# Optimization experiments

Hardware: AMD Instinct MI355X
Metric: run time of the kernel (lower is better)

The kernel has to match this reference:

```python
import jax, jax.numpy as jnp
import numpy as np

D = 384      # ViT-S feature dim (feat_dim_lookup['s'])
H = 6        # module forces num_heads = 6
L = 12       # ViT-S depth
RATIO = 0.1  # attention_mask_ratio
EPS = 1e-6


def layernorm(x, g, b):
    m = x.mean(-1, keepdims=True)
    v = ((x - m) ** 2).mean(-1, keepdims=True)
    return (x - m) * jax.lax.rsqrt(v + EPS) * g + b


def masked_attn(x, w_qkv, b_qkv, w_o, b_o):
    # Patch._fix_attn_masking: full softmax attention, threshold at ratio*row_max, renormalize.
    B, N, Dm = x.shape
    dh = Dm // H
    qkv = (x @ w_qkv + b_qkv).reshape(B, N, 3, H, dh)
    q = qkv[:, :, 0].transpose(0, 2, 1, 3)  # [B,H,N,dh]
    k = qkv[:, :, 1].transpose(0, 2, 1, 3)
    v = qkv[:, :, 2].transpose(0, 2, 1, 3)
    scores = jnp.einsum('bhqd,bhkd->bhqk', q, k) * (dh ** -0.5)
    attn = jax.nn.softmax(scores, axis=-1)
    thresh = RATIO * attn.max(axis=-1, keepdims=True)
    attn = jnp.where(attn >= thresh, attn, 0.0)
    attn = attn / attn.sum(axis=-1, keepdims=True)  # re-normalize
    out = jnp.einsum('bhqk,bhkd->bhqd', attn, v)
    out = out.transpose(0, 2, 1, 3).reshape(B, N, Dm)
    return out @ w_o + b_o, attn


def block(x, p):
    w_qkv, b_qkv, w_o, b_o, g1, be1, g2, be2, w1, b1, w2, b2 = p
    h, attn = masked_attn(layernorm(x, g1, be1), w_qkv, b_qkv, w_o, b_o)
    x = x + h
    h = layernorm(x, g2, be2) @ w1 + b1
    h = jax.nn.gelu(h, approximate=False) @ w2 + b2
    return x + h, attn


def setup_inputs() -> dict:
    key = jax.random.key(0)
    ks = jax.random.split(key, 8)
    B, N = 2, 962  # 2 transforms; (1+(160-8)//5)**2 + 1 cls = 962 tokens
    s = 0.02
    return {
        'x': jax.random.normal(ks[0], (B, N, D), jnp.float32),
        'w_qkv': jax.random.normal(ks[1], (L, D, 3 * D), jnp.float32) * s,
        'b_qkv': jnp.zeros((L, 3 * D), jnp.float32),
        'w_proj': jax.random.normal(ks[2], (L, D, D), jnp.float32) * s,
        'b_proj': jnp.zeros((L, D), jnp.float32),
        'ln1_g': jnp.ones((L, D), jnp.float32),
        'ln1_b': jnp.zeros((L, D), jnp.float32),
        'ln2_g': jnp.ones((L, D), jnp.float32),
        'ln2_b': jnp.zeros((L, D), jnp.float32),
        'w_fc1': jax.random.normal(ks[3], (L, D, 4 * D), jnp.float32) * s,
        'b_fc1': jnp.zeros((L, 4 * D), jnp.float32),
        'w_fc2': jax.random.normal(ks[4], (L, 4 * D, D), jnp.float32) * s,
        'b_fc2': jnp.zeros((L, D), jnp.float32),
        'lnf_g': jnp.ones((D,), jnp.float32),
        'lnf_b': jnp.zeros((D,), jnp.float32),
    }


def reference(x, w_qkv, b_qkv, w_proj, b_proj, ln1_g, ln1_b, ln2_g, ln2_b,
              w_fc1, b_fc1, w_fc2, b_fc2, lnf_g, lnf_b):
    params = (w_qkv, b_qkv, w_proj, b_proj, ln1_g, ln1_b, ln2_g, ln2_b,
              w_fc1, b_fc1, w_fc2, b_fc2)
    first = jax.tree_util.tree_map(lambda a: a[:-1], params)
    last = jax.tree_util.tree_map(lambda a: a[-1], params)

    def scan_fn(h, p):
        h, _ = block(h, p)
        return h, None

    x, _ = jax.lax.scan(scan_fn, x, first)  # blocks 0..L-2
    x, attn = block(x, last)                # last block, keep masked attention
    feats = layernorm(x, lnf_g, lnf_b)      # [B, N, D]
    return feats, attn
```

## Files before the change

kernel.cpp:

```cpp
#include <hip/hip_runtime.h>
#include <hip/hip_bf16.h>
#include <math.h>

typedef __bf16 bf16_t;
typedef __bf16 bf16x8 __attribute__((ext_vector_type(8)));
typedef __bf16 bf16x2 __attribute__((ext_vector_type(2)));
typedef float f32x4 __attribute__((ext_vector_type(4)));
typedef float f32x16 __attribute__((ext_vector_type(16)));

#define NEGBIG -3.0e38f

__global__ void __launch_bounds__(256) trall_k(
    const float* __restrict__ w_qkv, const float* __restrict__ w_proj,
    const float* __restrict__ w_fc1, const float* __restrict__ w_fc2,
    bf16_t* __restrict__ wt_qkv, bf16_t* __restrict__ wt_proj,
    bf16_t* __restrict__ wt_fc1, bf16_t* __restrict__ wt_fc2)
{
    __shared__ float T[32][33];
    int t = blockIdx.x;
    int z = t / 1728, r = t % 1728;
    const float* W; bf16_t* Wt; int K, N, n0, k0;
    if (r < 432)       { W = w_qkv;  Wt = wt_qkv;  K = 384;  N = 1152; n0 = (r % 36) * 32;               k0 = (r / 36) * 32; }
    else if (r < 576)  { W = w_proj; Wt = wt_proj; K = 384;  N = 384;  int rr = r - 432;  n0 = (rr % 12) * 32; k0 = (rr / 12) * 32; }
    else if (r < 1152) { W = w_fc1;  Wt = wt_fc1;  K = 384;  N = 1536; int rr = r - 576;  n0 = (rr % 48) * 32; k0 = (rr / 48) * 32; }
    else               { W = w_fc2;  Wt = wt_fc2;  K = 1536; N = 384;  int rr = r - 1152; n0 = (rr % 12) * 32; k0 = (rr / 12) * 32; }
    const float* Wl = W + (size_t)z * K * N;
    bf16_t* Wtl = Wt + (size_t)z * K * N;
    int tx = threadIdx.x & 31, ty = threadIdx.x >> 5;
#pragma unroll
    for (int i = 0; i < 4; ++i)
        T[ty + 8 * i][tx] = Wl[(size_t)(k0 + ty + 8 * i) * N + n0 + tx];
    __syncthreads();
#pragma unroll
    for (int i = 0; i < 4; ++i)
        Wtl[(size_t)(n0 + ty + 8 * i) * K + k0 + tx] = (bf16_t)T[tx][ty + 8 * i];
}

__global__ void __launch_bounds__(256) lncopy_k(
    const float* __restrict__ xin, const float* __restrict__ g,
    const float* __restrict__ b, float* __restrict__ xf,
    bf16_t* __restrict__ out)
{
    int t = blockIdx.x * 4 + (threadIdx.x >> 6);
    int lane = threadIdx.x & 63;
    const float* xp = xin + (size_t)t * 384;
    float v[6];
    float s = 0.f;
#pragma unroll
    for (int i = 0; i < 6; ++i) { v[i] = xp[lane + 64 * i]; s += v[i]; }
#pragma unroll
    for (int i = 0; i < 6; ++i) xf[(size_t)t * 384 + lane + 64 * i] = v[i];
    for (int off = 32; off > 0; off >>= 1) s += __shfl_xor(s, off);
    float mean = s * (1.0f / 384.0f);
    float s2 = 0.f;
#pragma unroll
    for (int i = 0; i < 6; ++i) { float d = v[i] - mean; s2 += d * d; }
    for (int off = 32; off > 0; off >>= 1) s2 += __shfl_xor(s2, off);
    float rstd = rsqrtf(s2 * (1.0f / 384.0f) + 1e-6f);
#pragma unroll
    for (int i = 0; i < 6; ++i) {
        int c = lane + 64 * i;
        out[(size_t)t * 384 + c] = (bf16_t)((v[i] - mean) * rstd * g[c] + b[c]);
    }
}

template <int NP, typename OT, bool WX>
__global__ void __launch_bounds__(256) ln_red_k(
    const float* __restrict__ x, const float* __restrict__ part,
    const float* __restrict__ g, const float* __restrict__ b,
    float* __restrict__ xupd, OT* __restrict__ out)
{
    int t = blockIdx.x * 4 + (threadIdx.x >> 6);
    int lane = threadIdx.x & 63;
    const size_t base = (size_t)t * 384;
    float v[6];
#pragma unroll
    for (int i = 0; i < 6; ++i) v[i] = x[base + lane + 64 * i];
#pragma unroll
    for (int p = 0; p < NP; ++p)
#pragma unroll
        for (int i = 0; i < 6; ++i)
            v[i] += part[(size_t)p * 738816 + base + lane + 64 * i];
    float s = 0.f;
#pragma unroll
    for (int i = 0; i < 6; ++i) {
        if (WX) xupd[base + lane + 64 * i] = v[i];
        s += v[i];
    }
    for (int off = 32; off > 0; off >>= 1) s += __shfl_xor(s, off);
    float mean = s * (1.0f / 384.0f);
    float s2 = 0.f;
#pragma unroll
    for (int i = 0; i < 6; ++i) { float d = v[i] - mean; s2 += d * d; }
    for (int off = 32; off > 0; off >>= 1) s2 += __shfl_xor(s2, off);
    float rstd = rsqrtf(s2 * (1.0f / 384.0f) + 1e-6f);
#pragma unroll
    for (int i = 0; i < 6; ++i) {
        int c = lane + 64 * i;
        out[base + c] = (OT)((v[i] - mean) * rstd * g[c] + b[c]);
    }
}

template <int MODE>
__global__ void __launch_bounds__(256) gemm_k(
    const bf16_t* __restrict__ A, const bf16_t* __restrict__ Bt,
    const float* __restrict__ bias, int M, int N, int K,
    bf16_t* __restrict__ outb,
    bf16_t* __restrict__ qb, bf16_t* __restrict__ kb, bf16_t* __restrict__ vtb)
{
    __shared__ alignas(16) bf16_t As[2][64][72];
    __shared__ alignas(16) bf16_t Bs[2][64][72];

    const int tid  = threadIdx.x;
    const int wave = tid >> 6, lane = tid & 63;
    const int m0 = blockIdx.y * 64, n0 = blockIdx.x * 64;
    const int rb = (wave >> 1) * 32, cb = (wave & 1) * 32;
    const int r32 = lane & 31, half = lane >> 5;
    const int h8 = half * 8;

    const int lrow = tid >> 3;
    const int lcol = (tid & 7) * 8;

    const bf16_t* pA0 = A  + (size_t)(m0 + lrow) * K + lcol;
    const bf16_t* pA1 = pA0 + (size_t)32 * K;
    const bf16_t* pB0 = Bt + (size_t)(n0 + lrow) * K + lcol;
    const bf16_t* pB1 = pB0 + (size_t)32 * K;

    f32x16 acc = {};
    bf16x8 va0, va1, vb0, vb1;

    va0 = *(const bf16x8*)(pA0);
    va1 = *(const bf16x8*)(pA1);
    vb0 = *(const bf16x8*)(pB0);
    vb1 = *(const bf16x8*)(pB1);
    *(bf16x8*)(&As[0][lrow][lcol])      = va0;
    *(bf16x8*)(&As[0][lrow + 32][lcol]) = va1;
    *(bf16x8*)(&Bs[0][lrow][lcol])      = vb0;
    *(bf16x8*)(&Bs[0][lrow + 32][lcol]) = vb1;

    int cur = 0;
    for (int k0 = 0; k0 < K; k0 += 64) {
        __syncthreads();
        const bool has_next = (k0 + 64 < K);
        if (has_next) {
            va0 = *(const bf16x8*)(pA0 + k0 + 64);
            va1 = *(const bf16x8*)(pA1 + k0 + 64);
            vb0 = *(const bf16x8*)(pB0 + k0 + 64);
            vb1 = *(const bf16x8*)(pB1 + k0 + 64);
        }
#pragma unroll
        for (int kc = 0; kc < 64; kc += 16) {
            bf16x8 a = *(const bf16x8*)(&As[cur][rb + r32][kc + h8]);
            bf16x8 b = *(const bf16x8*)(&Bs[cur][cb + r32][kc + h8]);
            acc = __builtin_amdgcn_mfma_f32_32x32x16_bf16(a, b, acc, 0, 0, 0);
        }
        if (has_next) {
            int nxt = cur ^ 1;
            *(bf16x8*)(&As[nxt][lrow][lcol])      = va0;
            *(bf16x8*)(&As[nxt][lrow + 32][lcol]) = va1;
            *(bf16x8*)(&Bs[nxt][lrow][lcol])      = vb0;
            *(bf16x8*)(&Bs[nxt][lrow + 32][lcol]) = vb1;
            cur = nxt;
        }
    }

    const int gc = n0 + cb + r32;
    const float bv = bias[gc];
    if (MODE == 2) {
#pragma unroll
        for (int reg = 0; reg < 16; ++reg) {
            int gr = m0 + rb + (reg & 3) + 8 * (reg >> 2) + 4 * half;
            if (gr >= M) continue;
            float val = acc[reg] + bv;
            float g = 0.5f * val * (1.0f + erff(val * 0.70710678118654752f));
            outb[(size_t)gr * N + gc] = (bf16_t)g;
        }
    } else {
        const int which = n0 / 384;
        if (which < 2) {
            const int rem = gc % 384;
            const int h = rem >> 6, d = rem & 63;
#pragma unroll
            for (int reg = 0; reg < 16; ++reg) {
                int gr = m0 + rb + (reg & 3) + 8 * (reg >> 2) + 4 * half;
                if (gr >= M) continue;
                float val = acc[reg] + bv;
                int bb = (gr >= 962) ? 1 : 0;
                int n = gr - 962 * bb;
                int bh = bb * 6 + h;
                bf16_t bvv = (bf16_t)val;
                if (which == 0) qb[((size_t)bh * 962 + n) * 64 + d] = bvv;
                else            kb[((size_t)bh * 962 + n) * 64 + d] = bvv;
            }
        } else {
            bf16_t (*T)[66] = (bf16_t (*)[66])(&As[0][0][0]);
            const int hh = (n0 - 768) >> 6;
            __syncthreads();
#pragma unroll
            for (int reg = 0; reg < 16; ++reg) {
                int rl = rb + (reg & 3) + 8 * (reg >> 2) + 4 * half;
                T[rl][cb + r32] = (bf16_t)(acc[reg] + bv);
            }
            __syncthreads();
            const int dl  = (wave << 4) + (lane >> 3);
            const int ncs = (lane & 7) * 8;
#pragma unroll
            for (int h8v = 0; h8v < 2; ++h8v) {
                int d = dl + h8v * 8;
                int ng0 = m0 + ncs;
                if (ng0 >= 1924) continue;
                bf16x8 v8;
#pragma unroll
                for (int j = 0; j < 8; ++j) v8[j] = T[ncs + j][d];
                int bb0 = (ng0 >= 962), bb7 = ((ng0 + 7) >= 962);
                if (bb0 == bb7 && ng0 + 7 < 1924) {
                    size_t off = ((size_t)(bb0 * 6 + hh) * 64 + d) * 992 + (ng0 - 962 * bb0);
                    if (bb0 == 0) {
                        *(bf16x8*)(vtb + off) = v8;
                    } else {
                        bf16x2* d2 = (bf16x2*)(vtb + off);
#pragma unroll
                        for (int j2 = 0; j2 < 4; ++j2) {
                            bf16x2 t2; t2[0] = v8[2 * j2]; t2[1] = v8[2 * j2 + 1];
                            d2[j2] = t2;
                        }
                    }
                } else {
                    for (int j = 0; j < 8; ++j) {
                        int ng = ng0 + j;
                        if (ng >= 1924) break;
                        int bb = (ng >= 962);
                        vtb[((size_t)(bb * 6 + hh) * 64 + d) * 992 + ng - 962 * bb] = v8[j];
                    }
                }
            }
        }
    }
}

template <int KLEN>
__global__ void __launch_bounds__(256) gemm_sp(
    const bf16_t* __restrict__ A, int lda,
    const bf16_t* __restrict__ Bt, int ldb,
    const float* __restrict__ bias, int M, int N,
    float* __restrict__ part)
{
    __shared__ alignas(16) bf16_t As[2][64][72];
    __shared__ alignas(16) bf16_t Bs[2][64][72];

    const int tid  = threadIdx.x;
    const int wave = tid >> 6, lane = tid & 63;
    const int m0 = blockIdx.y * 64, n0 = blockIdx.x * 64;
    const int rb = (wave >> 1) * 32, cb = (wave & 1) * 32;
    const int r32 = lane & 31, half = lane >> 5;
    const int h8 = half * 8;
    const int ks = blockIdx.z * KLEN;

    const int lrow = tid >> 3;
    const int lcol = (tid & 7) * 8;

    const bf16_t* pA0 = A  + (size_t)(m0 + lrow) * lda + ks + lcol;
    const bf16_t* pA1 = pA0 + (size_t)32 * lda;
    const bf16_t* pB0 = Bt + (size_t)(n0 + lrow) * ldb + ks + lcol;
    const bf16_t* pB1 = pB0 + (size_t)32 * ldb;

    f32x16 acc = {};
    bf16x8 va0, va1, vb0, vb1;

    va0 = *(const bf16x8*)(pA0);
    va1 = *(const bf16x8*)(pA1);
    vb0 = *(const bf16x8*)(pB0);
    vb1 = *(const bf16x8*)(pB1);
    *(bf16x8*)(&As[0][lrow][lcol])      = va0;
    *(bf16x8*)(&As[0][lrow + 32][lcol]) = va1;
    *(bf16x8*)(&Bs[0][lrow][lcol])      = vb0;
    *(bf16x8*)(&Bs[0][lrow + 32][lcol]) = vb1;

    int cur = 0;
    for (int k0 = 0; k0 < KLEN; k0 += 64) {
        __syncthreads();
        const bool has_next = (k0 + 64 < KLEN);
        if (has_next) {
            va0 = *(const bf16x8*)(pA0 + k0 + 64);
            va1 = *(const bf16x8*)(pA1 + k0 + 64);
            vb0 = *(const bf16x8*)(pB0 + k0 + 64);
            vb1 = *(const bf16x8*)(pB1 + k0 + 64);
        }
#pragma unroll
        for (int kc = 0; kc < 64; kc += 16) {
            bf16x8 a = *(const bf16x8*)(&As[cur][rb + r32][kc + h8]);
            bf16x8 b = *(const bf16x8*)(&Bs[cur][cb + r32][kc + h8]);
            acc = __builtin_amdgcn_mfma_f32_32x32x16_bf16(a, b, acc, 0, 0, 0);
        }
        if (has_next) {
            int nxt = cur ^ 1;
            *(bf16x8*)(&As[nxt][lrow][lcol])      = va0;
            *(bf16x8*)(&As[nxt][lrow + 32][lcol]) = va1;
            *(bf16x8*)(&Bs[nxt][lrow][lcol])      = vb0;
            *(bf16x8*)(&Bs[nxt][lrow + 32][lcol]) = vb1;
            cur = nxt;
        }
    }

    const int gc = n0 + cb + r32;
    const float bv = (blockIdx.z == 0) ? bias[gc] : 0.f;
    float* pz = part + (size_t)blockIdx.z * 738816;
#pragma unroll
    for (int reg = 0; reg < 16; ++reg) {
        int gr = m0 + rb + (reg & 3) + 8 * (reg >> 2) + 4 * half;
        if (gr >= M) continue;
        pz[(size_t)gr * N + gc] = acc[reg] + bv;
    }
}

__global__ void __launch_bounds__(256) attn_k(
    const bf16_t* __restrict__ qb, const bf16_t* __restrict__ kb,
    const bf16_t* __restrict__ vtb, bf16_t* __restrict__ attnout,
    float* __restrict__ attn_save)
{
    __shared__ alignas(16) bf16_t S[16][1000];

    const int tid  = threadIdx.x;
    const int wave = tid >> 6, lane = tid & 63;
    const int q4 = lane >> 4, mm = lane & 15;
    const int bh = blockIdx.y, qt = blockIdx.x;
    const int qrow0 = qt * 16;

    int qr = qrow0 + mm; if (qr > 961) qr = 961;
    const bf16_t* qptr = qb + ((size_t)bh * 962 + qr) * 64 + q4 * 8;
    bf16x8 aq0 = *(const bf16x8*)(qptr);
    bf16x8 aq1 = *(const bf16x8*)(qptr + 32);

    for (int ct = wave; ct < 61; ct += 4) {
        int kr = ct * 16 + mm; if (kr > 961) kr = 961;
        const bf16_t* kptr = kb + ((size_t)bh * 962 + kr) * 64 + q4 * 8;
        bf16x8 b0 = *(const bf16x8*)(kptr);
        bf16x8 b1 = *(const bf16x8*)(kptr + 32);
        f32x4 acc = {};
        acc = __builtin_amdgcn_mfma_f32_16x16x32_bf16(aq0, b0, acc, 0, 0, 0);
        acc = __builtin_amdgcn_mfma_f32_16x16x32_bf16(aq1, b1, acc, 0, 0, 0);
        int col = ct * 16 + mm;
#pragma unroll
        for (int r = 0; r < 4; ++r) {
            int row = q4 * 4 + r;
            if (col < 962) S[row][col] = (bf16_t)(acc[r] * 0.125f);
        }
    }
    for (int idx = tid; idx < 16 * 38; idx += 256) {
        int r = idx / 38, c = 962 + idx % 38;
        S[r][c] = (bf16_t)NEGBIG;
    }
    __syncthreads();

    const int trow = tid >> 4, ti = tid & 15;
    float e[8][8];
    float mx = NEGBIG;
#pragma unroll
    for (int t = 0; t < 8; ++t) {
        int c8 = ti * 8 + 128 * t;
        bf16x8 xv;
        if (c8 < 1000) xv = *(const bf16x8*)(&S[trow][c8]);
        else {
#pragma unroll
            for (int j = 0; j < 8; ++j) xv[j] = (bf16_t)NEGBIG;
        }
#pragma unroll
        for (int j = 0; j < 8; ++j) { e[t][j] = (float)xv[j]; mx = fmaxf(mx, e[t][j]); }
    }
#pragma unroll
    for (int off = 8; off > 0; off >>= 1) mx = fmaxf(mx, __shfl_xor(mx, off, 16));

    float sum = 0.f;
#pragma unroll
    for (int t = 0; t < 8; ++t)
#pragma unroll
    for (int j = 0; j < 8; ++j) {
        float ev = __expf(e[t][j] - mx);
        e[t][j] = ev;
        if (ev >= 0.1f) sum += ev;
    }
#pragma unroll
    for (int off = 8; off > 0; off >>= 1) sum += __shfl_xor(sum, off, 16);
    float inv = 1.0f / sum;

    int row_g = qrow0 + trow;
#pragma unroll
    for (int t = 0; t < 8; ++t) {
        int c8 = ti * 8 + 128 * t;
        if (c8 >= 1000) continue;
        bf16x8 pv;
#pragma unroll
        for (int j = 0; j < 8; ++j) {
            float pp = (e[t][j] >= 0.1f) ? e[t][j] * inv : 0.f;
            e[t][j] = pp;
            pv[j] = (bf16_t)pp;
        }
        *(bf16x8*)(&S[trow][c8]) = pv;
        if (attn_save && row_g < 962) {
#pragma unroll
            for (int j = 0; j < 8; ++j)
                if (c8 + j < 962)
                    attn_save[((size_t)bh * 962 + row_g) * 962 + c8 + j] = e[t][j];
        }
    }
    __syncthreads();

    const int wc0 = wave * 16;
    f32x4 o = {};
    for (int kc = 0; kc < 31; ++kc) {
        bf16x8 pa = *(const bf16x8*)(&S[mm][kc * 32 + q4 * 8]);
        bf16x8 vb = *(const bf16x8*)(vtb + ((size_t)bh * 64 + wc0 + mm) * 992 + kc * 32 + q4 * 8);
        o = __builtin_amdgcn_mfma_f32_16x16x32_bf16(pa, vb, o, 0, 0, 0);
    }
    int b = bh / 6, h = bh % 6;
#pragma unroll
    for (int r = 0; r < 4; ++r) {
        int qrr = qrow0 + q4 * 4 + r;
        if (qrr < 962)
            attnout[((size_t)(b * 962 + qrr)) * 384 + h * 64 + wc0 + mm] = (bf16_t)o[r];
    }
}

extern "C" void kernel_launch(void* const* d_in, const int* in_sizes, int n_in,
                              void* d_out, int out_size, void* d_ws, size_t ws_size,
                              hipStream_t stream)
{
    const float* xin    = (const float*)d_in[0];
    const float* w_qkv  = (const float*)d_in[1];
    const float* b_qkv  = (const float*)d_in[2];
    const float* w_proj = (const float*)d_in[3];
    const float* b_proj = (const float*)d_in[4];
    const float* ln1g   = (const float*)d_in[5];
    const float* ln1b   = (const float*)d_in[6];
    const float* ln2g   = (const float*)d_in[7];
    const float* ln2b   = (const float*)d_in[8];
    const float* w_fc1  = (const float*)d_in[9];
    const float* b_fc1  = (const float*)d_in[10];
    const float* w_fc2  = (const float*)d_in[11];
    const float* b_fc2  = (const float*)d_in[12];
    const float* lnfg   = (const float*)d_in[13];
    const float* lnfb   = (const float*)d_in[14];

    float* feats     = (float*)d_out;
    float* attn_save = feats + 738816;

    char* p = (char*)d_ws;
    auto alloc = [&](size_t bytes) {
        char* r = p;
        p += (bytes + 255) & ~(size_t)255;
        return r;
    };
    float*  x_f32   = (float*)alloc(1924ull * 384 * 4);
    bf16_t* xn      = (bf16_t*)alloc(1984ull * 384 * 2);
    bf16_t* qbuf    = (bf16_t*)alloc(12ull * 962 * 64 * 2);
    bf16_t* kbuf    = (bf16_t*)alloc(12ull * 962 * 64 * 2);
    bf16_t* vtbuf   = (bf16_t*)alloc(12ull * 64 * 992 * 2);
    bf16_t* attnout = (bf16_t*)alloc(1984ull * 384 * 2);
    bf16_t* mlp1    = (bf16_t*)alloc(1984ull * 1536 * 2);
    bf16_t* wt_qkv  = (bf16_t*)alloc(12ull * 1152 * 384 * 2);
    bf16_t* wt_proj = (bf16_t*)alloc(12ull * 384 * 384 * 2);
    bf16_t* wt_fc1  = (bf16_t*)alloc(12ull * 1536 * 384 * 2);
    bf16_t* wt_fc2  = (bf16_t*)alloc(12ull * 384 * 1536 * 2);
    float*  partbuf = (float*)alloc(4ull * 1924 * 384 * 4);

    trall_k<<<dim3(20736), dim3(256), 0, stream>>>(
        w_qkv, w_proj, w_fc1, w_fc2, wt_qkv, wt_proj, wt_fc1, wt_fc2);

    lncopy_k<<<dim3(481), dim3(256), 0, stream>>>(xin, ln1g, ln1b, x_f32, xn);

    for (int l = 0; l < 12; ++l) {
        gemm_k<0><<<dim3(18, 31), dim3(256), 0, stream>>>(
            xn, wt_qkv + (size_t)l * 1152 * 384, b_qkv + l * 1152,
            1924, 1152, 384, nullptr, qbuf, kbuf, vtbuf);
        attn_k<<<dim3(61, 12), dim3(256), 0, stream>>>(
            qbuf, kbuf, vtbuf, attnout, (l == 11) ? attn_save : (float*)nullptr);
        gemm_sp<192><<<dim3(6, 31, 2), dim3(256), 0, stream>>>(
            attnout, 384, wt_proj + (size_t)l * 384 * 384, 384, b_proj + l * 384,
            1924, 384, partbuf);
        ln_red_k<2, bf16_t, true><<<dim3(481), dim3(256), 0, stream>>>(
            x_f32, partbuf, ln2g + l * 384, ln2b + l * 384, x_f32, xn);
        gemm_k<2><<<dim3(24, 31), dim3(256), 0, stream>>>(
            xn, wt_fc1 + (size_t)l * 1536 * 384, b_fc1 + l * 1536,
            1924, 1536, 384, mlp1, nullptr, nullptr, nullptr);
        gemm_sp<384><<<dim3(6, 31, 4), dim3(256), 0, stream>>>(
            mlp1, 1536, wt_fc2 + (size_t)l * 384 * 1536, 1536, b_fc2 + l * 384,
            1924, 384, partbuf);
        if (l < 11) {
            ln_red_k<4, bf16_t, true><<<dim3(481), dim3(256), 0, stream>>>(
                x_f32, partbuf, ln1g + (l + 1) * 384, ln1b + (l + 1) * 384, x_f32, xn);
        } else {
            ln_red_k<4, float, false><<<dim3(481), dim3(256), 0, stream>>>(
                x_f32, partbuf, lnfg, lnfb, x_f32, feats);
        }
    }
}
```

Measured before the change: 966.0 us.

## Merge prep kernels, deepen GEMM register prefetch, vectorize attention-save stores

Folds the initial layernorm-copy kernel into the weight transpose kernel as extra blocks, saving one launch. Both GEMM kernels now prefetch global tiles two K-steps ahead using double register buffers, which gives loads more time to land behind the MFMA work. The attention-probability save in the last layer writes float pairs instead of scalars. The deeper prefetch raises register pressure, and the pair stores depend on row alignment, which holds because 962 is even.

```diff
diff --git a/kernel.cpp b/kernel.cpp
--- a/kernel.cpp
+++ b/kernel.cpp
@@ -5,17 +5,46 @@
 typedef __bf16 bf16_t;
 typedef __bf16 bf16x8 __attribute__((ext_vector_type(8)));
 typedef __bf16 bf16x2 __attribute__((ext_vector_type(2)));
+typedef float f32x2 __attribute__((ext_vector_type(2)));
 typedef float f32x4 __attribute__((ext_vector_type(4)));
 typedef float f32x16 __attribute__((ext_vector_type(16)));
 
 #define NEGBIG -3.0e38f
 
-__global__ void __launch_bounds__(256) trall_k(
+__global__ void __launch_bounds__(256) prep_k(
     const float* __restrict__ w_qkv, const float* __restrict__ w_proj,
     const float* __restrict__ w_fc1, const float* __restrict__ w_fc2,
     bf16_t* __restrict__ wt_qkv, bf16_t* __restrict__ wt_proj,
-    bf16_t* __restrict__ wt_fc1, bf16_t* __restrict__ wt_fc2)
+    bf16_t* __restrict__ wt_fc1, bf16_t* __restrict__ wt_fc2,
+    const float* __restrict__ xin, const float* __restrict__ g,
+    const float* __restrict__ b, float* __restrict__ xf,
+    bf16_t* __restrict__ xnout)
 {
+    if (blockIdx.x >= 20736) {
+        int t = (blockIdx.x - 20736) * 4 + (threadIdx.x >> 6);
+        int lane = threadIdx.x & 63;
+        const float* xp = xin + (size_t)t * 384;
+        float v[6];
+        float s = 0.f;
+#pragma unroll
+        for (int i = 0; i < 6; ++i) { v[i] = xp[lane + 64 * i]; s += v[i]; }
+#pragma unroll
+        for (int i = 0; i < 6; ++i) xf[(size_t)t * 384 + lane + 64 * i] = v[i];
+        for (int off = 32; off > 0; off >>= 1) s += __shfl_xor(s, off);
+        float mean = s * (1.0f / 384.0f);
+        float s2 = 0.f;
+#pragma unroll
+        for (int i = 0; i < 6; ++i) { float d = v[i] - mean; s2 += d * d; }
+        for (int off = 32; off > 0; off >>= 1) s2 += __shfl_xor(s2, off);
+        float rstd = rsqrtf(s2 * (1.0f / 384.0f) + 1e-6f);
+#pragma unroll
+        for (int i = 0; i < 6; ++i) {
+            int c = lane + 64 * i;
+            xnout[(size_t)t * 384 + c] = (bf16_t)((v[i] - mean) * rstd * g[c] + b[c]);
+        }
+        return;
+    }
+
     __shared__ float T[32][33];
     int t = blockIdx.x;
     int z = t / 1728, r = t % 1728;
@@ -36,34 +65,6 @@
         Wtl[(size_t)(n0 + ty + 8 * i) * K + k0 + tx] = (bf16_t)T[tx][ty + 8 * i];
 }
 
-__global__ void __launch_bounds__(256) lncopy_k(
-    const float* __restrict__ xin, const float* __restrict__ g,
-    const float* __restrict__ b, float* __restrict__ xf,
-    bf16_t* __restrict__ out)
-{
-    int t = blockIdx.x * 4 + (threadIdx.x >> 6);
-    int lane = threadIdx.x & 63;
-    const float* xp = xin + (size_t)t * 384;
-    float v[6];
-    float s = 0.f;
-#pragma unroll
-    for (int i = 0; i < 6; ++i) { v[i] = xp[lane + 64 * i]; s += v[i]; }
-#pragma unroll
-    for (int i = 0; i < 6; ++i) xf[(size_t)t * 384 + lane + 64 * i] = v[i];
-    for (int off = 32; off > 0; off >>= 1) s += __shfl_xor(s, off);
-    float mean = s * (1.0f / 384.0f);
-    float s2 = 0.f;
-#pragma unroll
-    for (int i = 0; i < 6; ++i) { float d = v[i] - mean; s2 += d * d; }
-    for (int off = 32; off > 0; off >>= 1) s2 += __shfl_xor(s2, off);
-    float rstd = rsqrtf(s2 * (1.0f / 384.0f) + 1e-6f);
-#pragma unroll
-    for (int i = 0; i < 6; ++i) {
-        int c = lane + 64 * i;
-        out[(size_t)t * 384 + c] = (bf16_t)((v[i] - mean) * rstd * g[c] + b[c]);
-    }
-}
-
 template <int NP, typename OT, bool WX>
 __global__ void __launch_bounds__(256) ln_red_k(
     const float* __restrict__ x, const float* __restrict__ part,
@@ -127,26 +128,33 @@
     const bf16_t* pB1 = pB0 + (size_t)32 * K;
 
     f32x16 acc = {};
-    bf16x8 va0, va1, vb0, vb1;
-
-    va0 = *(const bf16x8*)(pA0);
-    va1 = *(const bf16x8*)(pA1);
-    vb0 = *(const bf16x8*)(pB0);
-    vb1 = *(const bf16x8*)(pB1);
-    *(bf16x8*)(&As[0][lrow][lcol])      = va0;
-    *(bf16x8*)(&As[0][lrow + 32][lcol]) = va1;
-    *(bf16x8*)(&Bs[0][lrow][lcol])      = vb0;
-    *(bf16x8*)(&Bs[0][lrow + 32][lcol]) = vb1;
+    bf16x8 va0[2], va1[2], vb0[2], vb1[2];
+
+    va0[0] = *(const bf16x8*)(pA0);
+    va1[0] = *(const bf16x8*)(pA1);
+    vb0[0] = *(const bf16x8*)(pB0);
+    vb1[0] = *(const bf16x8*)(pB1);
+    if (64 < K) {
+        va0[1] = *(const bf16x8*)(pA0 + 64);
+        va1[1] = *(const bf16x8*)(pA1 + 64);
+        vb0[1] = *(const bf16x8*)(pB0 + 64);
+        vb1[1] = *(const bf16x8*)(pB1 + 64);
+    }
+    *(bf16x8*)(&As[0][lrow][lcol])      = va0[0];
+    *(bf16x8*)(&As[0][lrow + 32][lcol]) = va1[0];
+    *(bf16x8*)(&Bs[0][lrow][lcol])      = vb0[0];
+    *(bf16x8*)(&Bs[0][lrow + 32][lcol]) = vb1[0];
 
     int cur = 0;
-    for (int k0 = 0; k0 < K; k0 += 64) {
+    int i = 0;
+    for (int k0 = 0; k0 < K; k0 += 64, ++i) {
         __syncthreads();
-        const bool has_next = (k0 + 64 < K);
-        if (has_next) {
-            va0 = *(const bf16x8*)(pA0 + k0 + 64);
-            va1 = *(const bf16x8*)(pA1 + k0 + 64);
-            vb0 = *(const bf16x8*)(pB0 + k0 + 64);
-            vb1 = *(const bf16x8*)(pB1 + k0 + 64);
+        const int s = i & 1;
+        if (k0 + 128 < K) {
+            va0[s] = *(const bf16x8*)(pA0 + k0 + 128);
+            va1[s] = *(const bf16x8*)(pA1 + k0 + 128);
+            vb0[s] = *(const bf16x8*)(pB0 + k0 + 128);
+            vb1[s] = *(const bf16x8*)(pB1 + k0 + 128);
         }
 #pragma unroll
         for (int kc = 0; kc < 64; kc += 16) {
@@ -154,12 +162,13 @@
             bf16x8 b = *(const bf16x8*)(&Bs[cur][cb + r32][kc + h8]);
             acc = __builtin_amdgcn_mfma_f32_32x32x16_bf16(a, b, acc, 0, 0, 0);
         }
-        if (has_next) {
+        if (k0 + 64 < K) {
+            const int ns = s ^ 1;
             int nxt = cur ^ 1;
-            *(bf16x8*)(&As[nxt][lrow][lcol])      = va0;
-            *(bf16x8*)(&As[nxt][lrow + 32][lcol]) = va1;
-            *(bf16x8*)(&Bs[nxt][lrow][lcol])      = vb0;
-            *(bf16x8*)(&Bs[nxt][lrow + 32][lcol]) = vb1;
+            *(bf16x8*)(&As[nxt][lrow][lcol])      = va0[ns];
+            *(bf16x8*)(&As[nxt][lrow + 32][lcol]) = va1[ns];
+            *(bf16x8*)(&Bs[nxt][lrow][lcol])      = vb0[ns];
+            *(bf16x8*)(&Bs[nxt][lrow + 32][lcol]) = vb1[ns];
             cur = nxt;
         }
     }
@@ -265,26 +274,33 @@
     const bf16_t* pB1 = pB0 + (size_t)32 * ldb;
 
     f32x16 acc = {};
-    bf16x8 va0, va1, vb0, vb1;
-
-    va0 = *(const bf16x8*)(pA0);
-    va1 = *(const bf16x8*)(pA1);
-    vb0 = *(const bf16x8*)(pB0);
-    vb1 = *(const bf16x8*)(pB1);
-    *(bf16x8*)(&As[0][lrow][lcol])      = va0;
-    *(bf16x8*)(&As[0][lrow + 32][lcol]) = va1;
-    *(bf16x8*)(&Bs[0][lrow][lcol])      = vb0;
-    *(bf16x8*)(&Bs[0][lrow + 32][lcol]) = vb1;
+    bf16x8 va0[2], va1[2], vb0[2], vb1[2];
+
+    va0[0] = *(const bf16x8*)(pA0);
+    va1[0] = *(const bf16x8*)(pA1);
+    vb0[0] = *(const bf16x8*)(pB0);
+    vb1[0] = *(const bf16x8*)(pB1);
+    if (64 < KLEN) {
+        va0[1] = *(const bf16x8*)(pA0 + 64);
+        va1[1] = *(const bf16x8*)(pA1 + 64);
+        vb0[1] = *(const bf16x8*)(pB0 + 64);
+        vb1[1] = *(const bf16x8*)(pB1 + 64);
+    }
+    *(bf16x8*)(&As[0][lrow][lcol])      = va0[0];
+    *(bf16x8*)(&As[0][lrow + 32][lcol]) = va1[0];
+    *(bf16x8*)(&Bs[0][lrow][lcol])      = vb0[0];
+    *(bf16x8*)(&Bs[0][lrow + 32][lcol]) = vb1[0];
 
     int cur = 0;
-    for (int k0 = 0; k0 < KLEN; k0 += 64) {
+    int i = 0;
+    for (int k0 = 0; k0 < KLEN; k0 += 64, ++i) {
         __syncthreads();
-        const bool has_next = (k0 + 64 < KLEN);
-        if (has_next) {
-            va0 = *(const bf16x8*)(pA0 + k0 + 64);
-            va1 = *(const bf16x8*)(pA1 + k0 + 64);
-            vb0 = *(const bf16x8*)(pB0 + k0 + 64);
-            vb1 = *(const bf16x8*)(pB1 + k0 + 64);
+        const int s = i & 1;
+        if (k0 + 128 < KLEN) {
+            va0[s] = *(const bf16x8*)(pA0 + k0 + 128);
+            va1[s] = *(const bf16x8*)(pA1 + k0 + 128);
+            vb0[s] = *(const bf16x8*)(pB0 + k0 + 128);
+            vb1[s] = *(const bf16x8*)(pB1 + k0 + 128);
         }
 #pragma unroll
         for (int kc = 0; kc < 64; kc += 16) {
@@ -292,12 +308,13 @@
             bf16x8 b = *(const bf16x8*)(&Bs[cur][cb + r32][kc + h8]);
             acc = __builtin_amdgcn_mfma_f32_32x32x16_bf16(a, b, acc, 0, 0, 0);
         }
-        if (has_next) {
+        if (k0 + 64 < KLEN) {
+            const int ns = s ^ 1;
             int nxt = cur ^ 1;
-            *(bf16x8*)(&As[nxt][lrow][lcol])      = va0;
-            *(bf16x8*)(&As[nxt][lrow + 32][lcol]) = va1;
-            *(bf16x8*)(&Bs[nxt][lrow][lcol])      = vb0;
-            *(bf16x8*)(&Bs[nxt][lrow + 32][lcol]) = vb1;
+            *(bf16x8*)(&As[nxt][lrow][lcol])      = va0[ns];
+            *(bf16x8*)(&As[nxt][lrow + 32][lcol]) = va1[ns];
+            *(bf16x8*)(&Bs[nxt][lrow][lcol])      = vb0[ns];
+            *(bf16x8*)(&Bs[nxt][lrow + 32][lcol]) = vb1[ns];
             cur = nxt;
         }
     }
@@ -397,10 +414,17 @@
         }
         *(bf16x8*)(&S[trow][c8]) = pv;
         if (attn_save && row_g < 962) {
-#pragma unroll
-            for (int j = 0; j < 8; ++j)
-                if (c8 + j < 962)
-                    attn_save[((size_t)bh * 962 + row_g) * 962 + c8 + j] = e[t][j];
+            float* dst = attn_save + ((size_t)bh * 962 + row_g) * 962 + c8;
+            if (c8 + 8 <= 962) {
+#pragma unroll
+                for (int j2 = 0; j2 < 4; ++j2) {
+                    f32x2 t2; t2[0] = e[t][2 * j2]; t2[1] = e[t][2 * j2 + 1];
+                    *(f32x2*)(dst + 2 * j2) = t2;
+                }
+            } else {
+                for (int j = 0; j < 8; ++j)
+                    if (c8 + j < 962) dst[j] = e[t][j];
+            }
         }
     }
     __syncthreads();
@@ -463,10 +487,9 @@
     bf16_t* wt_fc2  = (bf16_t*)alloc(12ull * 384 * 1536 * 2);
     float*  partbuf = (float*)alloc(4ull * 1924 * 384 * 4);
 
-    trall_k<<<dim3(20736), dim3(256), 0, stream>>>(
-        w_qkv, w_proj, w_fc1, w_fc2, wt_qkv, wt_proj, wt_fc1, wt_fc2);
-
-    lncopy_k<<<dim3(481), dim3(256), 0, stream>>>(xin, ln1g, ln1b, x_f32, xn);
+    prep_k<<<dim3(21217), dim3(256), 0, stream>>>(
+        w_qkv, w_proj, w_fc1, w_fc2, wt_qkv, wt_proj, wt_fc1, wt_fc2,
+        xin, ln1g, ln1b, x_f32, xn);
 
     for (int l = 0; l < 12; ++l) {
         gemm_k<0><<<dim3(18, 31), dim3(256), 0, stream>>>(
```

After: 1.657 ms. +71.5%, slower.
